# Performance work log

Hardware: AMD Instinct MI355X
Metric: run time of the kernel (lower is better)

Reference implementation:

```python
import jax, jax.numpy as jnp
import numpy as np

L, R, H = 4, 4, 16          # left heads, right heads, per-head hidden
D = L * H                    # 64 = left*h = right*h = output_size
B, T = 2, 96


def setup_inputs() -> dict:
    key = jax.random.key(0)
    ks = jax.random.split(key, 16)
    p = lambda k, s: jax.random.normal(k, s, dtype=jnp.float32) * 0.1
    return {
        "queries": jax.random.normal(ks[0], (B, T, D, D), dtype=jnp.float32),
        "keys":    jax.random.normal(ks[1], (B, T, D, D), dtype=jnp.float32),
        "values":  jax.random.normal(ks[2], (B, T, D, D), dtype=jnp.float32),
        "Wq_row": p(ks[3], (D, D)), "Wq_col": p(ks[4], (D, D)), "bq": p(ks[5], (D, D)),
        "Wk_row": p(ks[6], (D, D)), "Wk_col": p(ks[7], (D, D)), "bk": p(ks[8], (D, D)),
        "Wv_row": p(ks[9], (D, D)), "Wv_col": p(ks[10], (D, D)), "bv": p(ks[11], (D, D)),
        "Wo_row": p(ks[12], (D, D)), "Wo_col": p(ks[13], (D, D)), "bo": p(ks[14], (D, D)),
    }


def _pdense(x, Wr, Wc, b):
    # PartialDenseLayer: dense transform on BOTH trailing axes of the 2D token
    # [..., i, j] -> [..., a, b]
    return jnp.einsum('...ij,ia,jb->...ab', x, Wr, Wc) + b


def _separate(x):
    # [B, T, L*H, R*H] -> [B, T, L, R, H, H]
    b, t = x.shape[:2]
    return x.reshape(b, t, L, H, R, H).transpose(0, 1, 2, 4, 3, 5)


def _merge(x):
    # [B, T, L, R, H, H] -> [B, T, L*H, R*H]
    b, t = x.shape[:2]
    return x.transpose(0, 1, 2, 4, 3, 5).reshape(b, t, L * H, R * H)


def reference(queries, keys, values,
              Wq_row, Wq_col, bq, Wk_row, Wk_col, bk,
              Wv_row, Wv_col, bv, Wo_row, Wo_col, bo):
    h = float(H)
    q = _separate(_pdense(queries, Wq_row, Wq_col, bq) / h)  # [B,Tq,L,R,H,H]
    k = _separate(_pdense(keys,    Wk_row, Wk_col, bk) / h)  # [B,Tk,L,R,H,H]
    v = _separate(_pdense(values,  Wv_row, Wv_col, bv) / h)  # [B,Tk,L,R,H,H]
    # similarity_method (method_one): q @ k^T on trailing HxH matrices
    logits = jnp.einsum('bilrpm,bjlrqm->bijlrpq', q, k) / h  # [B,Tq,Tk,L,R,H,H]
    w = jax.nn.softmax(logits, axis=2)                        # softmax over key axis (-5)
    # causal ordering mask over the (L, R) head grid (band_part lower-tri)
    mask = jnp.tril(jnp.ones((L, R), dtype=w.dtype))
    w = w * mask[None, None, None, :, :, None, None]
    # merge_method (method_one): matmul with values then sum over keys
    out = jnp.einsum('bijlrpm,bjlrmq->bilrpq', w, v)          # [B,Tq,L,R,H,H]
    return _pdense(_merge(out), Wo_row, Wo_col, bo) / h       # [B,Tq,D,D]
```

## Files before the change

### kernel.cpp

```cpp
#include <hip/hip_runtime.h>
#include <hip/hip_bf16.h>
#include <math.h>

typedef unsigned int uint32;
typedef unsigned short ushort_t;
typedef __attribute__((ext_vector_type(8))) short s8v;
typedef __attribute__((ext_vector_type(16))) float f16v;
typedef __attribute__((ext_vector_type(2))) unsigned int u2v;

#define LH 4
#define RH 4
#define DD 64
#define BB 2
#define TT 96
#define NTOK (BB*TT)
#define HEADS 16
#define VHEADS 10
#define INV_H 0.0625f
#define LOG2E 1.4426950408889634f
#define QKV_BLOCKS 288
#define ZF_BLOCKS 48

struct U2 { uint32 x, y; };
struct U4 { uint32 x, y, z, w; };

__device__ __forceinline__ uint32 f2bf(float f) {
    return (uint32)__builtin_bit_cast(ushort_t, __float2bfloat16(f));
}
__device__ __forceinline__ uint32 pkbf(float lo, float hi) {
    return f2bf(lo) | (f2bf(hi) << 16);
}
__device__ __forceinline__ float bf2f(uint32 u) {
    return __uint_as_float(u << 16);
}
__device__ __forceinline__ void hswap(uint32 &a, uint32 &b, int h) {
#if __has_builtin(__builtin_amdgcn_permlane32_swap)
    u2v rr = __builtin_amdgcn_permlane32_swap(a, b, false, false);
    a = rr.x; b = rr.y;
#else
    uint32 xa = (uint32)__shfl_xor((int)a, 32, 64);
    uint32 xb = (uint32)__shfl_xor((int)b, 32, 64);
    uint32 na = (h == 0) ? xb : a;
    uint32 nb = (h == 0) ? b  : xa;
    a = na; b = nb;
#endif
}

__global__ __launch_bounds__(256) void wprep_kernel(
    const float* __restrict__ Wq_row, const float* __restrict__ Wq_col, const float* __restrict__ bq,
    const float* __restrict__ Wk_row, const float* __restrict__ Wk_col, const float* __restrict__ bk,
    const float* __restrict__ Wv_row, const float* __restrict__ Wv_col, const float* __restrict__ bv,
    const float* __restrict__ Wo_row, const float* __restrict__ Wo_col, const float* __restrict__ bo,
    ushort_t* __restrict__ wct, ushort_t* __restrict__ wrt, float* __restrict__ bT)
{
    const int task = blockIdx.x;
    const int tid = threadIdx.x;
    #pragma unroll
    for (int e = 0; e < 16; ++e) {
        const int idx = e * 256 + tid;
        const int src = (idx & 63) * 64 + (idx >> 6);
        switch (task) {
        case 0: wct[idx]          = (ushort_t)f2bf(Wq_col[src]); break;
        case 1: wct[4096 + idx]   = (ushort_t)f2bf(Wk_col[src]); break;
        case 2: wct[8192 + idx]   = (ushort_t)f2bf(Wv_col[src]); break;
        case 3: wrt[idx]          = (ushort_t)f2bf(Wq_row[src]); break;
        case 4: wrt[4096 + idx]   = (ushort_t)f2bf(Wk_row[src]); break;
        case 5: wrt[8192 + idx]   = (ushort_t)f2bf(Wv_row[src]); break;
        case 6: bT[idx]           = bq[src]; break;
        case 7: bT[4096 + idx]    = bk[src]; break;
        default: bT[8192 + idx]   = bv[src]; break;
        }
    }
}

__global__ __launch_bounds__(256) void pdense_qkv_mfma(
    const float* __restrict__ Xq, const float* __restrict__ Xk, const float* __restrict__ Xv,
    const ushort_t* __restrict__ wct, const ushort_t* __restrict__ wrt,
    const float* __restrict__ bT,
    ushort_t* __restrict__ q_bf, ushort_t* __restrict__ k_bf,
    ushort_t* __restrict__ vt_bf, float* __restrict__ att)
{
    __shared__ float lds_t1[4][32][68];

    const int bid = blockIdx.x;
    if (bid >= QKV_BLOCKS) {
        const int zb = bid - QKV_BLOCKS;
        float4* a4 = (float4*)att;
        #pragma unroll
        for (int it = 0; it < 16; ++it)
            a4[(size_t)zb * 4096 + it * 256 + threadIdx.x] = float4{0.f, 0.f, 0.f, 0.f};
        return;
    }
    const int wv = threadIdx.x >> 6;
    const int task = bid * 4 + wv;
    const int proj = task / (NTOK * 2);
    const int rem  = task % (NTOK * 2);
    const int token = rem >> 1;
    const int ch = rem & 1;
    const int lane = threadIdx.x & 63;
    const int c5 = lane & 31, h = lane >> 5;
    const int c = ch * 32 + c5;
    const int bI = token / TT, t = token % TT;

    const float* X = (proj == 0) ? Xq : (proj == 1) ? Xk : Xv;
    const float* Xp = X + (size_t)token * 4096;
    const ushort_t* wc = wct + proj * 4096;
    const ushort_t* wr = wrt + proj * 4096;
    const float*    bt = bT + proj * 4096;
    const float scale = (proj == 0) ? (INV_H * INV_H * LOG2E) : INV_H;

    const f16v fz = {0,0,0,0,0,0,0,0,0,0,0,0,0,0,0,0};

    f16v t1_0 = fz, t1_1 = fz;
    #pragma unroll
    for (int n = 0; n < 4; ++n) {
        s8v bf = *(const s8v*)(wc + c * 64 + n * 16 + 8 * h);
        {
            const float* xr = Xp + (size_t)c5 * 64 + n * 16 + 8 * h;
            float4 xa = *(const float4*)xr, xb = *(const float4*)(xr + 4);
            U4 u = { pkbf(xa.x, xa.y), pkbf(xa.z, xa.w), pkbf(xb.x, xb.y), pkbf(xb.z, xb.w) };
            t1_0 = __builtin_amdgcn_mfma_f32_32x32x16_bf16(__builtin_bit_cast(s8v, u), bf, t1_0, 0, 0, 0);
        }
        {
            const float* xr = Xp + (size_t)(32 + c5) * 64 + n * 16 + 8 * h;
            float4 xa = *(const float4*)xr, xb = *(const float4*)(xr + 4);
            U4 u = { pkbf(xa.x, xa.y), pkbf(xa.z, xa.w), pkbf(xb.x, xb.y), pkbf(xb.z, xb.w) };
            t1_1 = __builtin_amdgcn_mfma_f32_32x32x16_bf16(__builtin_bit_cast(s8v, u), bf, t1_1, 0, 0, 0);
        }
    }

    #pragma unroll
    for (int tt = 0; tt < 16; ++tt) {
        const int i = (tt & 3) + 8 * (tt >> 2) + 4 * h;
        lds_t1[wv][c5][i]      = t1_0[tt];
        lds_t1[wv][c5][32 + i] = t1_1[tt];
    }
    __syncthreads();

    s8v bfr[4];
    #pragma unroll
    for (int n = 0; n < 4; ++n) {
        const float* p = &lds_t1[wv][c5][n * 16 + 8 * h];
        float4 xa = *(const float4*)p, xb = *(const float4*)(p + 4);
        U4 u = { pkbf(xa.x, xa.y), pkbf(xa.z, xa.w), pkbf(xb.x, xb.y), pkbf(xb.z, xb.w) };
        bfr[n] = __builtin_bit_cast(s8v, u);
    }

    #pragma unroll
    for (int At = 0; At < 2; ++At) {
        f16v y = fz;
        #pragma unroll
        for (int n = 0; n < 4; ++n) {
            s8v af = *(const s8v*)(wr + (size_t)(32 * At + c5) * 64 + n * 16 + 8 * h);
            y = __builtin_amdgcn_mfma_f32_32x32x16_bf16(af, bfr[n], y, 0, 0, 0);
        }
        #pragma unroll
        for (int rg = 0; rg < 4; ++rg) {
            float4 bv = *(const float4*)(bt + c * 64 + 32 * At + 8 * rg + 4 * h);
            float be[4] = {bv.x, bv.y, bv.z, bv.w};
            #pragma unroll
            for (int e = 0; e < 4; ++e) {
                const int a = 32 * At + 8 * rg + 4 * h + e;
                const float val = (y[rg * 4 + e] + be[e]) * scale;
                const ushort_t ov = (ushort_t)f2bf(val);
                const size_t base =
                    ((size_t)((bI * HEADS + (a >> 4) * RH + (c >> 4)) * TT + t)) * 256;
                if (proj == 0)      q_bf[base + (a & 15) * 16 + (c & 15)] = ov;
                else if (proj == 1) k_bf[base + (a & 15) * 16 + (c & 15)] = ov;
                else                vt_bf[base + (c & 15) * 16 + (a & 15)] = ov;
            }
        }
    }
}

__global__ __launch_bounds__(128, 2) void pdense_out_fp32(
    const float* __restrict__ Xall, const float* __restrict__ Wr,
    const float* __restrict__ Wc, const float* __restrict__ bias,
    float* __restrict__ dst)
{
    __shared__ float XsT[64 * 68];
    __shared__ float T1r[64 * 36];

    const int token = blockIdx.x >> 1, half = blockIdx.x & 1;
    const float* Xp = Xall + (size_t)token * 4096;

    const int tid = threadIdx.x;
    const int g4 = tid >> 3;
    const int cq = tid & 7;
    const int c0 = half * 32 + cq * 4;

    #pragma unroll
    for (int rep = 0; rep < 32; ++rep) {
        int idx = tid + rep * 128;
        int i = idx >> 6, j = idx & 63;
        XsT[j * 68 + i] = Xp[idx];
    }
    __syncthreads();

    {
        const float4* X4 = (const float4*)XsT;
        float4 a0 = {0,0,0,0}, a1 = {0,0,0,0}, a2 = {0,0,0,0}, a3 = {0,0,0,0};
        #pragma unroll 8
        for (int j = 0; j < 64; ++j) {
            float4 xv = X4[j * 17 + g4];
            float4 wv = *(const float4*)&Wc[j * 64 + c0];
            a0.x = fmaf(xv.x, wv.x, a0.x); a0.y = fmaf(xv.x, wv.y, a0.y);
            a0.z = fmaf(xv.x, wv.z, a0.z); a0.w = fmaf(xv.x, wv.w, a0.w);
            a1.x = fmaf(xv.y, wv.x, a1.x); a1.y = fmaf(xv.y, wv.y, a1.y);
            a1.z = fmaf(xv.y, wv.z, a1.z); a1.w = fmaf(xv.y, wv.w, a1.w);
            a2.x = fmaf(xv.z, wv.x, a2.x); a2.y = fmaf(xv.z, wv.y, a2.y);
            a2.z = fmaf(xv.z, wv.z, a2.z); a2.w = fmaf(xv.z, wv.w, a2.w);
            a3.x = fmaf(xv.w, wv.x, a3.x); a3.y = fmaf(xv.w, wv.y, a3.y);
            a3.z = fmaf(xv.w, wv.z, a3.z); a3.w = fmaf(xv.w, wv.w, a3.w);
        }
        *(float4*)&T1r[(g4 * 4 + 0) * 36 + cq * 4] = a0;
        *(float4*)&T1r[(g4 * 4 + 1) * 36 + cq * 4] = a1;
        *(float4*)&T1r[(g4 * 4 + 2) * 36 + cq * 4] = a2;
        *(float4*)&T1r[(g4 * 4 + 3) * 36 + cq * 4] = a3;
    }
    __syncthreads();

    float4 y0 = {0,0,0,0}, y1 = {0,0,0,0}, y2 = {0,0,0,0}, y3 = {0,0,0,0};
    #pragma unroll 8
    for (int i = 0; i < 64; ++i) {
        float4 wv = *(const float4*)&Wr[i * 64 + g4 * 4];
        float4 tv = *(const float4*)&T1r[i * 36 + cq * 4];
        y0.x = fmaf(wv.x, tv.x, y0.x); y0.y = fmaf(wv.x, tv.y, y0.y);
        y0.z = fmaf(wv.x, tv.z, y0.z); y0.w = fmaf(wv.x, tv.w, y0.w);
        y1.x = fmaf(wv.y, tv.x, y1.x); y1.y = fmaf(wv.y, tv.y, y1.y);
        y1.z = fmaf(wv.y, tv.z, y1.z); y1.w = fmaf(wv.y, tv.w, y1.w);
        y2.x = fmaf(wv.z, tv.x, y2.x); y2.y = fmaf(wv.z, tv.y, y2.y);
        y2.z = fmaf(wv.z, tv.z, y2.z); y2.w = fmaf(wv.z, tv.w, y2.w);
        y3.x = fmaf(wv.w, tv.x, y3.x); y3.y = fmaf(wv.w, tv.y, y3.y);
        y3.z = fmaf(wv.w, tv.z, y3.z); y3.w = fmaf(wv.w, tv.w, y3.w);
    }

    float4 ys[4] = {y0, y1, y2, y3};
    #pragma unroll
    for (int aa = 0; aa < 4; ++aa) {
        int a = g4 * 4 + aa;
        float4 bv = *(const float4*)&bias[a * 64 + c0];
        float4 v;
        v.x = (ys[aa].x + bv.x) * INV_H; v.y = (ys[aa].y + bv.y) * INV_H;
        v.z = (ys[aa].z + bv.z) * INV_H; v.w = (ys[aa].w + bv.w) * INV_H;
        *(float4*)(dst + (size_t)token * 4096 + a * 64 + c0) = v;
    }
}

__global__ __launch_bounds__(256, 4) void attn_kernel(
    const ushort_t* __restrict__ q_bf,
    const ushort_t* __restrict__ k_bf,
    const ushort_t* __restrict__ vt_bf,
    float* __restrict__ att)
{
    __shared__ float lds_z[4][64][9];
    __shared__ float lds_pv[4][64][17];

    const int ip = blockIdx.x % (TT / 2);
    const int vh = (blockIdx.x / (TT / 2)) % VHEADS;
    const int bI = blockIdx.x / ((TT / 2) * VHEADS);
    const int l = (vh >= 1) + (vh >= 3) + (vh >= 6);
    const int r = vh - (l * (l + 1)) / 2;
    const int head = l * RH + r;
    const int i0 = ip * 2;
    const int lane = threadIdx.x & 63;
    const int wv = threadIdx.x >> 6;
    const int c5 = lane & 31;
    const int h  = lane >> 5;

    const size_t hb = (size_t)(bI * HEADS + head) * TT * 256;
    const int frow = (c5 & 15) * 16 + 8 * h;

    s8v qf = *(const s8v*)(q_bf + hb + (size_t)(i0 + (c5 >> 4)) * 256 + frow);
    const ushort_t* kb = k_bf + hb + frow;
    const ushort_t* vb = vt_bf + hb + frow;

    const int jb = wv * (TT / 4);
    const f16v fz16 = {0,0,0,0,0,0,0,0,0,0,0,0,0,0,0,0};

    float ls[8] = {0,0,0,0,0,0,0,0};
    #pragma unroll 3
    for (int jp = 0; jp < 12; ++jp) {
        const int j0g = jb + jp * 2;
        s8v kf = *(const s8v*)(kb + (size_t)(j0g + (c5 >> 4)) * 256);
        f16v d = __builtin_amdgcn_mfma_f32_32x32x16_bf16(kf, qf, fz16, 0, 0, 0);
        #pragma unroll
        for (int t = 0; t < 8; ++t)
            ls[t] += exp2f(d[t]) + exp2f(d[t + 8]);
    }
    #pragma unroll
    for (int t = 0; t < 8; ++t) lds_z[wv][lane][t] = ls[t];
    __syncthreads();
    float inv[8];
    #pragma unroll
    for (int t = 0; t < 8; ++t) {
        float s = lds_z[0][lane][t] + lds_z[1][lane][t]
                + lds_z[2][lane][t] + lds_z[3][lane][t];
        inv[t] = 1.f / s;
    }

    f16v pv = fz16;
    #pragma unroll 2
    for (int jp = 0; jp < 12; ++jp) {
        const int j0g = jb + jp * 2;
        s8v kf = *(const s8v*)(kb + (size_t)(j0g + (c5 >> 4)) * 256);
        f16v d = __builtin_amdgcn_mfma_f32_32x32x16_bf16(kf, qf, fz16, 0, 0, 0);
        float w[16];
        #pragma unroll
        for (int t = 0; t < 8; ++t) {
            w[t]     = exp2f(d[t])     * inv[t];
            w[t + 8] = exp2f(d[t + 8]) * inv[t];
        }
        uint32 A0 = pkbf(w[0],  w[1]),  A1 = pkbf(w[2],  w[3]);
        uint32 A2 = pkbf(w[4],  w[5]),  A3 = pkbf(w[6],  w[7]);
        uint32 B0 = pkbf(w[8],  w[9]),  B1 = pkbf(w[10], w[11]);
        uint32 B2 = pkbf(w[12], w[13]), B3 = pkbf(w[14], w[15]);
        hswap(A2, A0, h); hswap(A3, A1, h);
        hswap(B2, B0, h); hswap(B3, B1, h);
        U4 fa = {A0, A1, A2, A3};
        U4 fb = {B0, B1, B2, B3};
        s8v vf0 = *(const s8v*)(vb + (size_t)(j0g + 0) * 256);
        s8v vf1 = *(const s8v*)(vb + (size_t)(j0g + 1) * 256);
        pv = __builtin_amdgcn_mfma_f32_32x32x16_bf16(__builtin_bit_cast(s8v, fa), vf0, pv, 0, 0, 0);
        pv = __builtin_amdgcn_mfma_f32_32x32x16_bf16(__builtin_bit_cast(s8v, fb), vf1, pv, 0, 0, 0);
    }

    #pragma unroll
    for (int t = 0; t < 16; ++t) lds_pv[wv][lane][t] = pv[t];
    __syncthreads();

    if (c5 < 16) {
        #pragma unroll
        for (int rr = 0; rr < 4; ++rr) {
            const int reg = wv * 4 + rr;
            float v = lds_pv[0][lane][reg] + lds_pv[1][lane][reg]
                    + lds_pv[2][lane][reg] + lds_pv[3][lane][reg];
            const int row = rr + 8 * wv + 4 * h;
            const int i = row >> 4, p = row & 15;
            att[((size_t)(bI * TT + i0 + i) * DD + l * 16 + p) * DD + r * 16 + c5] = v;
        }
    }
}

extern "C" void kernel_launch(void* const* d_in, const int* in_sizes, int n_in,
                              void* d_out, int out_size, void* d_ws, size_t ws_size,
                              hipStream_t stream) {
    const float* queries = (const float*)d_in[0];
    const float* keys    = (const float*)d_in[1];
    const float* values  = (const float*)d_in[2];
    const float* Wq_row  = (const float*)d_in[3];
    const float* Wq_col  = (const float*)d_in[4];
    const float* bq      = (const float*)d_in[5];
    const float* Wk_row  = (const float*)d_in[6];
    const float* Wk_col  = (const float*)d_in[7];
    const float* bk      = (const float*)d_in[8];
    const float* Wv_row  = (const float*)d_in[9];
    const float* Wv_col  = (const float*)d_in[10];
    const float* bv      = (const float*)d_in[11];
    const float* Wo_row  = (const float*)d_in[12];
    const float* Wo_col  = (const float*)d_in[13];
    const float* bo      = (const float*)d_in[14];
    float* out = (float*)d_out;

    const size_t SEP = (size_t)BB * HEADS * TT * 256;
    ushort_t* q_bf  = (ushort_t*)d_ws;
    ushort_t* k_bf  = q_bf + SEP;
    ushort_t* vt_bf = k_bf + SEP;
    float*    att   = (float*)(vt_bf + SEP);
    ushort_t* wct   = (ushort_t*)(att + SEP);
    ushort_t* wrt   = wct + 3 * 4096;
    float*    bT    = (float*)(wrt + 3 * 4096);

    wprep_kernel<<<9, 256, 0, stream>>>(
        Wq_row, Wq_col, bq, Wk_row, Wk_col, bk, Wv_row, Wv_col, bv,
        Wo_row, Wo_col, bo, wct, wrt, bT);

    pdense_qkv_mfma<<<QKV_BLOCKS + ZF_BLOCKS, 256, 0, stream>>>(
        queries, keys, values, wct, wrt, bT, q_bf, k_bf, vt_bf, att);

    attn_kernel<<<BB * VHEADS * (TT / 2), 256, 0, stream>>>(q_bf, k_bf, vt_bf, att);

    pdense_out_fp32<<<NTOK * 2, 128, 0, stream>>>(att, Wo_row, Wo_col, bo, out);
}
```

Measured before the change: 65.09 us.

## Move output partial-dense layer to bf16x3 split-precision MFMA

```diff
diff --git a/kernel.cpp b/kernel.cpp
--- a/kernel.cpp
+++ b/kernel.cpp
@@ -33,6 +33,11 @@
 __device__ __forceinline__ float bf2f(uint32 u) {
     return __uint_as_float(u << 16);
 }
+__device__ __forceinline__ void hl_pair(float v0, float v1, uint32 &hw, uint32 &lw) {
+    uint32 h0 = f2bf(v0), h1 = f2bf(v1);
+    hw = h0 | (h1 << 16);
+    lw = pkbf(v0 - bf2f(h0), v1 - bf2f(h1));
+}
 __device__ __forceinline__ void hswap(uint32 &a, uint32 &b, int h) {
 #if __has_builtin(__builtin_amdgcn_permlane32_swap)
     u2v rr = __builtin_amdgcn_permlane32_swap(a, b, false, false);
@@ -51,7 +56,10 @@
     const float* __restrict__ Wk_row, const float* __restrict__ Wk_col, const float* __restrict__ bk,
     const float* __restrict__ Wv_row, const float* __restrict__ Wv_col, const float* __restrict__ bv,
     const float* __restrict__ Wo_row, const float* __restrict__ Wo_col, const float* __restrict__ bo,
-    ushort_t* __restrict__ wct, ushort_t* __restrict__ wrt, float* __restrict__ bT)
+    ushort_t* __restrict__ wct, ushort_t* __restrict__ wrt, float* __restrict__ bT,
+    ushort_t* __restrict__ woct_h, ushort_t* __restrict__ woct_l,
+    ushort_t* __restrict__ wort_h, ushort_t* __restrict__ wort_l,
+    float* __restrict__ boT)
 {
     const int task = blockIdx.x;
     const int tid = threadIdx.x;
@@ -68,7 +76,20 @@
         case 5: wrt[8192 + idx]   = (ushort_t)f2bf(Wv_row[src]); break;
         case 6: bT[idx]           = bq[src]; break;
         case 7: bT[4096 + idx]    = bk[src]; break;
-        default: bT[8192 + idx]   = bv[src]; break;
+        case 8: bT[8192 + idx]    = bv[src]; break;
+        case 9: {
+            float v = Wo_col[src];
+            uint32 hh = f2bf(v);
+            woct_h[idx] = (ushort_t)hh;
+            woct_l[idx] = (ushort_t)f2bf(v - bf2f(hh));
+            break; }
+        case 10: {
+            float v = Wo_row[src];
+            uint32 hh = f2bf(v);
+            wort_h[idx] = (ushort_t)hh;
+            wort_l[idx] = (ushort_t)f2bf(v - bf2f(hh));
+            break; }
+        default: boT[idx] = bo[src]; break;
         }
     }
 }
@@ -173,77 +194,92 @@
     }
 }
 
-__global__ __launch_bounds__(128, 2) void pdense_out_fp32(
-    const float* __restrict__ Xall, const float* __restrict__ Wr,
-    const float* __restrict__ Wc, const float* __restrict__ bias,
-    float* __restrict__ dst)
+__global__ __launch_bounds__(256) void pdense_out_mfma2(
+    const float* __restrict__ att,
+    const ushort_t* __restrict__ woct_h, const ushort_t* __restrict__ woct_l,
+    const ushort_t* __restrict__ wort_h, const ushort_t* __restrict__ wort_l,
+    const float* __restrict__ boT, float* __restrict__ out)
 {
-    __shared__ float XsT[64 * 68];
-    __shared__ float T1r[64 * 36];
-
-    const int token = blockIdx.x >> 1, half = blockIdx.x & 1;
-    const float* Xp = Xall + (size_t)token * 4096;
-
-    const int tid = threadIdx.x;
-    const int g4 = tid >> 3;
-    const int cq = tid & 7;
-    const int c0 = half * 32 + cq * 4;
-
-    #pragma unroll
-    for (int rep = 0; rep < 32; ++rep) {
-        int idx = tid + rep * 128;
-        int i = idx >> 6, j = idx & 63;
-        XsT[j * 68 + i] = Xp[idx];
+    __shared__ float lds_t1[4][32][68];
+
+    const int wv = threadIdx.x >> 6;
+    const int task = blockIdx.x * 4 + wv;
+    const int token = task >> 1, ch = task & 1;
+    const int lane = threadIdx.x & 63;
+    const int c5 = lane & 31, h = lane >> 5;
+    const int c = ch * 32 + c5;
+
+    const float* Xp = att + (size_t)token * 4096;
+    const f16v fz = {0,0,0,0,0,0,0,0,0,0,0,0,0,0,0,0};
+
+    f16v t1_0 = fz, t1_1 = fz;
+    #pragma unroll
+    for (int n = 0; n < 4; ++n) {
+        s8v bh = *(const s8v*)(woct_h + c * 64 + n * 16 + 8 * h);
+        s8v bl = *(const s8v*)(woct_l + c * 64 + n * 16 + 8 * h);
+        #pragma unroll
+        for (int T = 0; T < 2; ++T) {
+            const float* xr = Xp + (size_t)(32 * T + c5) * 64 + n * 16 + 8 * h;
+            float4 xa = *(const float4*)xr, xb = *(const float4*)(xr + 4);
+            uint32 hw0, lw0, hw1, lw1, hw2, lw2, hw3, lw3;
+            hl_pair(xa.x, xa.y, hw0, lw0);
+            hl_pair(xa.z, xa.w, hw1, lw1);
+            hl_pair(xb.x, xb.y, hw2, lw2);
+            hl_pair(xb.z, xb.w, hw3, lw3);
+            U4 uh = {hw0, hw1, hw2, hw3}, ul = {lw0, lw1, lw2, lw3};
+            s8v ah = __builtin_bit_cast(s8v, uh), al = __builtin_bit_cast(s8v, ul);
+            f16v acc = (T == 0) ? t1_0 : t1_1;
+            acc = __builtin_amdgcn_mfma_f32_32x32x16_bf16(ah, bh, acc, 0, 0, 0);
+            acc = __builtin_amdgcn_mfma_f32_32x32x16_bf16(al, bh, acc, 0, 0, 0);
+            acc = __builtin_amdgcn_mfma_f32_32x32x16_bf16(ah, bl, acc, 0, 0, 0);
+            if (T == 0) t1_0 = acc; else t1_1 = acc;
+        }
+    }
+
+    #pragma unroll
+    for (int tt = 0; tt < 16; ++tt) {
+        const int i = (tt & 3) + 8 * (tt >> 2) + 4 * h;
+        lds_t1[wv][c5][i]      = t1_0[tt];
+        lds_t1[wv][c5][32 + i] = t1_1[tt];
     }
     __syncthreads();
 
-    {
-        const float4* X4 = (const float4*)XsT;
-        float4 a0 = {0,0,0,0}, a1 = {0,0,0,0}, a2 = {0,0,0,0}, a3 = {0,0,0,0};
-        #pragma unroll 8
-        for (int j = 0; j < 64; ++j) {
-            float4 xv = X4[j * 17 + g4];
-            float4 wv = *(const float4*)&Wc[j * 64 + c0];
-            a0.x = fmaf(xv.x, wv.x, a0.x); a0.y = fmaf(xv.x, wv.y, a0.y);
-            a0.z = fmaf(xv.x, wv.z, a0.z); a0.w = fmaf(xv.x, wv.w, a0.w);
-            a1.x = fmaf(xv.y, wv.x, a1.x); a1.y = fmaf(xv.y, wv.y, a1.y);
-            a1.z = fmaf(xv.y, wv.z, a1.z); a1.w = fmaf(xv.y, wv.w, a1.w);
-            a2.x = fmaf(xv.z, wv.x, a2.x); a2.y = fmaf(xv.z, wv.y, a2.y);
-            a2.z = fmaf(xv.z, wv.z, a2.z); a2.w = fmaf(xv.z, wv.w, a2.w);
-            a3.x = fmaf(xv.w, wv.x, a3.x); a3.y = fmaf(xv.w, wv.y, a3.y);
-            a3.z = fmaf(xv.w, wv.z, a3.z); a3.w = fmaf(xv.w, wv.w, a3.w);
-        }
-        *(float4*)&T1r[(g4 * 4 + 0) * 36 + cq * 4] = a0;
-        *(float4*)&T1r[(g4 * 4 + 1) * 36 + cq * 4] = a1;
-        *(float4*)&T1r[(g4 * 4 + 2) * 36 + cq * 4] = a2;
-        *(float4*)&T1r[(g4 * 4 + 3) * 36 + cq * 4] = a3;
-    }
-    __syncthreads();
-
-    float4 y0 = {0,0,0,0}, y1 = {0,0,0,0}, y2 = {0,0,0,0}, y3 = {0,0,0,0};
-    #pragma unroll 8
-    for (int i = 0; i < 64; ++i) {
-        float4 wv = *(const float4*)&Wr[i * 64 + g4 * 4];
-        float4 tv = *(const float4*)&T1r[i * 36 + cq * 4];
-        y0.x = fmaf(wv.x, tv.x, y0.x); y0.y = fmaf(wv.x, tv.y, y0.y);
-        y0.z = fmaf(wv.x, tv.z, y0.z); y0.w = fmaf(wv.x, tv.w, y0.w);
-        y1.x = fmaf(wv.y, tv.x, y1.x); y1.y = fmaf(wv.y, tv.y, y1.y);
-        y1.z = fmaf(wv.y, tv.z, y1.z); y1.w = fmaf(wv.y, tv.w, y1.w);
-        y2.x = fmaf(wv.z, tv.x, y2.x); y2.y = fmaf(wv.z, tv.y, y2.y);
-        y2.z = fmaf(wv.z, tv.z, y2.z); y2.w = fmaf(wv.z, tv.w, y2.w);
-        y3.x = fmaf(wv.w, tv.x, y3.x); y3.y = fmaf(wv.w, tv.y, y3.y);
-        y3.z = fmaf(wv.w, tv.z, y3.z); y3.w = fmaf(wv.w, tv.w, y3.w);
-    }
-
-    float4 ys[4] = {y0, y1, y2, y3};
-    #pragma unroll
-    for (int aa = 0; aa < 4; ++aa) {
-        int a = g4 * 4 + aa;
-        float4 bv = *(const float4*)&bias[a * 64 + c0];
-        float4 v;
-        v.x = (ys[aa].x + bv.x) * INV_H; v.y = (ys[aa].y + bv.y) * INV_H;
-        v.z = (ys[aa].z + bv.z) * INV_H; v.w = (ys[aa].w + bv.w) * INV_H;
-        *(float4*)(dst + (size_t)token * 4096 + a * 64 + c0) = v;
+    s8v bfh[4], bfl[4];
+    #pragma unroll
+    for (int n = 0; n < 4; ++n) {
+        const float* p = &lds_t1[wv][c5][n * 16 + 8 * h];
+        float4 xa = *(const float4*)p, xb = *(const float4*)(p + 4);
+        uint32 h0, l0, h1, l1, h2, l2, h3, l3;
+        hl_pair(xa.x, xa.y, h0, l0);
+        hl_pair(xa.z, xa.w, h1, l1);
+        hl_pair(xb.x, xb.y, h2, l2);
+        hl_pair(xb.z, xb.w, h3, l3);
+        U4 uh = {h0, h1, h2, h3}, ul = {l0, l1, l2, l3};
+        bfh[n] = __builtin_bit_cast(s8v, uh);
+        bfl[n] = __builtin_bit_cast(s8v, ul);
+    }
+
+    #pragma unroll
+    for (int At = 0; At < 2; ++At) {
+        f16v y = fz;
+        #pragma unroll
+        for (int n = 0; n < 4; ++n) {
+            s8v awh = *(const s8v*)(wort_h + (size_t)(32 * At + c5) * 64 + n * 16 + 8 * h);
+            s8v awl = *(const s8v*)(wort_l + (size_t)(32 * At + c5) * 64 + n * 16 + 8 * h);
+            y = __builtin_amdgcn_mfma_f32_32x32x16_bf16(awh, bfh[n], y, 0, 0, 0);
+            y = __builtin_amdgcn_mfma_f32_32x32x16_bf16(awh, bfl[n], y, 0, 0, 0);
+            y = __builtin_amdgcn_mfma_f32_32x32x16_bf16(awl, bfh[n], y, 0, 0, 0);
+        }
+        #pragma unroll
+        for (int rg = 0; rg < 4; ++rg) {
+            float4 bv = *(const float4*)(boT + c * 64 + 32 * At + 8 * rg + 4 * h);
+            float be[4] = {bv.x, bv.y, bv.z, bv.w};
+            #pragma unroll
+            for (int e = 0; e < 4; ++e) {
+                const int a = 32 * At + 8 * rg + 4 * h + e;
+                out[(size_t)token * 4096 + a * 64 + c] = (y[rg * 4 + e] + be[e]) * INV_H;
+            }
+        }
     }
 }
 
@@ -367,18 +403,25 @@
     ushort_t* k_bf  = q_bf + SEP;
     ushort_t* vt_bf = k_bf + SEP;
     float*    att   = (float*)(vt_bf + SEP);
-    ushort_t* wct   = (ushort_t*)(att + SEP);
-    ushort_t* wrt   = wct + 3 * 4096;
-    float*    bT    = (float*)(wrt + 3 * 4096);
-
-    wprep_kernel<<<9, 256, 0, stream>>>(
+    ushort_t* wct    = (ushort_t*)(att + SEP);
+    ushort_t* wrt    = wct + 3 * 4096;
+    float*    bT     = (float*)(wrt + 3 * 4096);
+    ushort_t* woct_h = (ushort_t*)(bT + 3 * 4096);
+    ushort_t* woct_l = woct_h + 4096;
+    ushort_t* wort_h = woct_l + 4096;
+    ushort_t* wort_l = wort_h + 4096;
+    float*    boT    = (float*)(wort_l + 4096);
+
+    wprep_kernel<<<12, 256, 0, stream>>>(
         Wq_row, Wq_col, bq, Wk_row, Wk_col, bk, Wv_row, Wv_col, bv,
-        Wo_row, Wo_col, bo, wct, wrt, bT);
+        Wo_row, Wo_col, bo,
+        wct, wrt, bT, woct_h, woct_l, wort_h, wort_l, boT);
 
     pdense_qkv_mfma<<<QKV_BLOCKS + ZF_BLOCKS, 256, 0, stream>>>(
         queries, keys, values, wct, wrt, bT, q_bf, k_bf, vt_bf, att);
 
     attn_kernel<<<BB * VHEADS * (TT / 2), 256, 0, stream>>>(q_bf, k_bf, vt_bf, att);
 
-    pdense_out_fp32<<<NTOK * 2, 128, 0, stream>>>(att, Wo_row, Wo_col, bo, out);
-}
+    pdense_out_mfma2<<<NTOK * 2 / 4, 256, 0, stream>>>(
+        att, woct_h, woct_l, wort_h, wort_l, boT, out);
+}
```

New measurement: 62.51 us. -4.0%, faster.
